# Optimization experiments

Measured on AMD Instinct MI355X. Metric: run time of the kernel, lower is better.

## Reference

```python
import jax, jax.numpy as jnp
import numpy as np

N_NODES = 50000
N_EDGES = 600000
D = 128
OUT = 16


def setup_inputs() -> dict:
    key = jax.random.key(0)
    k1, k2, k3, k4, k5, k6 = jax.random.split(key, 6)
    hn = jax.random.normal(k1, (N_NODES, D), dtype=jnp.float32)
    he = jax.random.normal(k2, (N_EDGES, D), dtype=jnp.float32)
    src = jax.random.randint(k3, (N_EDGES,), 0, N_NODES, dtype=jnp.int64)
    dst = jax.random.randint(k4, (N_EDGES,), 0, N_NODES, dtype=jnp.int64)
    W = jax.random.normal(k5, (OUT, 3 * D), dtype=jnp.float32) * 0.05
    b = jax.random.normal(k6, (OUT,), dtype=jnp.float32) * 0.05
    return {"hn": hn, "he": he, "src": src, "dst": dst, "W": W, "b": b}


def reference(hn, he, src, dst, W, b):
    # gather source/dest node features per edge, concat with edge feature
    h_u = hn[src]                      # [E, D]
    h_v = hn[dst]                      # [E, D]
    cat = jnp.concatenate([h_u, h_v, he], axis=1)  # [E, 3D]
    score = cat @ W.T + b              # [E, OUT]
    return score
```

## Files before the change

### kernel.cpp

```cpp
#include <hip/hip_runtime.h>
#include <hip/hip_bf16.h>


#define D      128
#define OUT    16
#define KTOT   384
#define KSTEPS 12

typedef __attribute__((ext_vector_type(8))) short  short8;
typedef __attribute__((ext_vector_type(4))) float  float4v;

__device__ __forceinline__ unsigned short f2bf(float x) {
    unsigned u = __builtin_bit_cast(unsigned, x);
    unsigned r = u + 0x7fffu + ((u >> 16) & 1u);
    return (unsigned short)(r >> 16);
}

__device__ __forceinline__ short8 load_cvt8(const float* __restrict__ p) {
    float4v a = *(const float4v*)(p);
    float4v c = *(const float4v*)(p + 4);
    short8 r;
#pragma unroll
    for (int i = 0; i < 4; ++i) {
        r[i]     = (short)f2bf(a[i]);
        r[i + 4] = (short)f2bf(c[i]);
    }
    return r;
}

__global__ __launch_bounds__(256) void egat_mfma_kernel(
    const float* __restrict__ hn,
    const float* __restrict__ he,
    const int*   __restrict__ src,
    const int*   __restrict__ dst,
    const float* __restrict__ W,
    const float* __restrict__ b,
    float*       __restrict__ out,
    int n_tiles, int total_waves)
{
    const int wave = (blockIdx.x * blockDim.x + threadIdx.x) >> 6;
    const int lane = threadIdx.x & 63;
    const int l    = lane & 15;
    const int quad = lane >> 4;
    const int off  = quad * 8;

    short8 wf[KSTEPS];
    const float* wrow = W + l * KTOT;
#pragma unroll
    for (int s = 0; s < KSTEPS; ++s)
        wf[s] = load_cvt8(wrow + s * 32 + off);

    const float bias = b[l];

    for (int tile = wave; tile < n_tiles; tile += total_waves) {
        const int e  = tile * 16 + l;
        const int su = src[e];
        const int dv = dst[e];
        const float* ru = hn + (size_t)su * D;
        const float* rv = hn + (size_t)dv * D;
        const float* re = he + (size_t)e  * D;

        float4v acc = {0.f, 0.f, 0.f, 0.f};
#pragma unroll
        for (int s = 0; s < 4; ++s) {
            short8 af = load_cvt8(ru + s * 32 + off);
            acc = __builtin_amdgcn_mfma_f32_16x16x32_bf16(af, wf[s], acc, 0, 0, 0);
        }
#pragma unroll
        for (int s = 0; s < 4; ++s) {
            short8 af = load_cvt8(rv + s * 32 + off);
            acc = __builtin_amdgcn_mfma_f32_16x16x32_bf16(af, wf[4 + s], acc, 0, 0, 0);
        }
#pragma unroll
        for (int s = 0; s < 4; ++s) {
            short8 af = load_cvt8(re + s * 32 + off);
            acc = __builtin_amdgcn_mfma_f32_16x16x32_bf16(af, wf[8 + s], acc, 0, 0, 0);
        }

        const size_t ebase = (size_t)tile * 16;
#pragma unroll
        for (int i = 0; i < 4; ++i) {
            int row = quad * 4 + i;
            out[(ebase + row) * OUT + l] = acc[i] + bias;
        }
    }
}

extern "C" void kernel_launch(void* const* d_in, const int* in_sizes, int n_in,
                              void* d_out, int out_size, void* d_ws, size_t ws_size,
                              hipStream_t stream) {
    const float* hn  = (const float*)d_in[0];
    const float* he  = (const float*)d_in[1];
    const int*   src = (const int*)d_in[2];
    const int*   dst = (const int*)d_in[3];
    const float* W   = (const float*)d_in[4];
    const float* b   = (const float*)d_in[5];
    float* out = (float*)d_out;

    const int E = in_sizes[2];
    const int n_tiles = E / 16;
    const int blocks = 1875;
    const int total_waves = blocks * 4;

    egat_mfma_kernel<<<blocks, 256, 0, stream>>>(hn, he, src, dst, W, b, out,
                                                 n_tiles, total_waves);
}
```

Baseline: 491.2 us.

## Stream edge features via async global-to-LDS copies and stage W in LDS

Each wave now copies its 16 contiguous edge-feature rows into padded LDS with asynchronous global_load_lds while it gathers and multiplies the node features. The next tile's src/dst indices are prefetched, and W is converted to bf16 once per block and held in LDS instead of registers. The grid becomes contiguous chunks of three tiles per wave. The aim is coalesced he loads, overlap of memory latency with MFMA work, and lower register pressure; the costs are LDS traffic for W and a hand-coded waitcnt whose correctness depends on the vmcnt encoding.

Result: faster. 475.9 us (-3.1%).

```diff
diff --git a/kernel.cpp b/kernel.cpp
--- a/kernel.cpp
+++ b/kernel.cpp
@@ -5,7 +5,10 @@
 #define D      128
 #define OUT    16
 #define KTOT   384
-#define KSTEPS 12
+#define HE_ROW_B   528
+#define HE_ROW_F   132
+#define HE_WAVE_F  2304
+#define W_ROW_S    392
 
 typedef __attribute__((ext_vector_type(8))) short  short8;
 typedef __attribute__((ext_vector_type(4))) float  float4v;
@@ -16,9 +19,7 @@
     return (unsigned short)(r >> 16);
 }
 
-__device__ __forceinline__ short8 load_cvt8(const float* __restrict__ p) {
-    float4v a = *(const float4v*)(p);
-    float4v c = *(const float4v*)(p + 4);
+__device__ __forceinline__ short8 cvt8(float4v a, float4v c) {
     short8 r;
 #pragma unroll
     for (int i = 0; i < 4; ++i) {
@@ -26,6 +27,12 @@
         r[i + 4] = (short)f2bf(c[i]);
     }
     return r;
+}
+
+__device__ __forceinline__ void async_copy16(const float* g, float* lds) {
+    __builtin_amdgcn_global_load_lds(
+        (const __attribute__((address_space(1))) void*)g,
+        (__attribute__((address_space(3))) void*)lds, 16, 0, 0);
 }
 
 __global__ __launch_bounds__(256) void egat_mfma_kernel(
@@ -36,53 +43,99 @@
     const float* __restrict__ W,
     const float* __restrict__ b,
     float*       __restrict__ out,
-    int n_tiles, int total_waves)
+    int n_tiles, int tiles_per_wave)
 {
-    const int wave = (blockIdx.x * blockDim.x + threadIdx.x) >> 6;
-    const int lane = threadIdx.x & 63;
+    __shared__ __align__(16) unsigned short w_lds[16 * W_ROW_S];
+    __shared__ __align__(16) float he_lds[4 * HE_WAVE_F];
+
+    const int tid  = threadIdx.x;
+    const int wib  = tid >> 6;
+    const int lane = tid & 63;
     const int l    = lane & 15;
     const int quad = lane >> 4;
     const int off  = quad * 8;
 
-    short8 wf[KSTEPS];
-    const float* wrow = W + l * KTOT;
+    for (int i = tid; i < 16 * KTOT; i += 256) {
+        int row = i / KTOT, col = i - row * KTOT;
+        w_lds[row * W_ROW_S + col] = f2bf(W[i]);
+    }
+    __syncthreads();
+
+    int goff[9];
 #pragma unroll
-    for (int s = 0; s < KSTEPS; ++s)
-        wf[s] = load_cvt8(wrow + s * 32 + off);
+    for (int j = 0; j < 9; ++j) {
+        int x = j * 1024 + lane * 16;
+        int r = x / HE_ROW_B;
+        int c = x - r * HE_ROW_B;
+        goff[j] = (r < 16 && c < 512) ? (r * 512 + c) >> 2 : 0;
+    }
 
     const float bias = b[l];
+    float* hb = &he_lds[wib * HE_WAVE_F];
 
-    for (int tile = wave; tile < n_tiles; tile += total_waves) {
-        const int e  = tile * 16 + l;
-        const int su = src[e];
-        const int dv = dst[e];
+    const int wave  = (blockIdx.x * 4) + wib;
+    const int tile0 = wave * tiles_per_wave;
+
+    int e0 = tile0 * 16 + l;
+    int su = src[e0];
+    int dv = dst[e0];
+
+    for (int i = 0; i < tiles_per_wave; ++i) {
+        const int tile = tile0 + i;
+        if (tile >= n_tiles) break;
+
+        const float* hp = he + (size_t)tile * (16 * D);
+#pragma unroll
+        for (int j = 0; j < 9; ++j)
+            async_copy16(hp + goff[j], hb + j * 256);
+
+        int tn = tile + 1; if (tn >= n_tiles) tn = n_tiles - 1;
+        const int en = tn * 16 + l;
+        const int su_n = src[en];
+        const int dv_n = dst[en];
+
         const float* ru = hn + (size_t)su * D;
         const float* rv = hn + (size_t)dv * D;
-        const float* re = he + (size_t)e  * D;
+        float4v au[8], av[8];
+#pragma unroll
+        for (int s = 0; s < 4; ++s) {
+            au[2 * s]     = *(const float4v*)(ru + s * 32 + off);
+            au[2 * s + 1] = *(const float4v*)(ru + s * 32 + off + 4);
+            av[2 * s]     = *(const float4v*)(rv + s * 32 + off);
+            av[2 * s + 1] = *(const float4v*)(rv + s * 32 + off + 4);
+        }
 
         float4v acc = {0.f, 0.f, 0.f, 0.f};
 #pragma unroll
         for (int s = 0; s < 4; ++s) {
-            short8 af = load_cvt8(ru + s * 32 + off);
-            acc = __builtin_amdgcn_mfma_f32_16x16x32_bf16(af, wf[s], acc, 0, 0, 0);
+            short8 wf = *(const short8*)&w_lds[l * W_ROW_S + s * 32 + off];
+            acc = __builtin_amdgcn_mfma_f32_16x16x32_bf16(
+                      cvt8(au[2 * s], au[2 * s + 1]), wf, acc, 0, 0, 0);
         }
 #pragma unroll
         for (int s = 0; s < 4; ++s) {
-            short8 af = load_cvt8(rv + s * 32 + off);
-            acc = __builtin_amdgcn_mfma_f32_16x16x32_bf16(af, wf[4 + s], acc, 0, 0, 0);
+            short8 wf = *(const short8*)&w_lds[l * W_ROW_S + (4 + s) * 32 + off];
+            acc = __builtin_amdgcn_mfma_f32_16x16x32_bf16(
+                      cvt8(av[2 * s], av[2 * s + 1]), wf, acc, 0, 0, 0);
         }
+
+        __builtin_amdgcn_s_waitcnt(0x0F70);
+
 #pragma unroll
         for (int s = 0; s < 4; ++s) {
-            short8 af = load_cvt8(re + s * 32 + off);
-            acc = __builtin_amdgcn_mfma_f32_16x16x32_bf16(af, wf[8 + s], acc, 0, 0, 0);
+            const int fi = l * HE_ROW_F + s * 32 + off;
+            float4v ha = *(const float4v*)&hb[fi];
+            float4v hc = *(const float4v*)&hb[fi + 4];
+            short8 wf = *(const short8*)&w_lds[l * W_ROW_S + (8 + s) * 32 + off];
+            acc = __builtin_amdgcn_mfma_f32_16x16x32_bf16(cvt8(ha, hc), wf, acc, 0, 0, 0);
         }
 
         const size_t ebase = (size_t)tile * 16;
 #pragma unroll
-        for (int i = 0; i < 4; ++i) {
-            int row = quad * 4 + i;
-            out[(ebase + row) * OUT + l] = acc[i] + bias;
-        }
+        for (int r = 0; r < 4; ++r)
+            out[(ebase + quad * 4 + r) * OUT + l] = acc[r] + bias;
+
+        su = su_n; dv = dv_n;
     }
 }
 
@@ -98,10 +151,11 @@
     float* out = (float*)d_out;
 
     const int E = in_sizes[2];
-    const int n_tiles = E / 16;
-    const int blocks = 1875;
-    const int total_waves = blocks * 4;
+    const int n_tiles = (E + 15) / 16;
+    const int tiles_per_wave = 3;
+    const int waves = (n_tiles + tiles_per_wave - 1) / tiles_per_wave;
+    const int blocks = (waves + 3) / 4;
 
     egat_mfma_kernel<<<blocks, 256, 0, stream>>>(hn, he, src, dst, W, b, out,
-                                                 n_tiles, total_waves);
+                                                 n_tiles, tiles_per_wave);
 }
```

## Precompute per-node projections, then gather projected scores per edge

Applied to the files above, without the earlier changes.

Splits the linear layer so each node's features are projected once through the src and dst slices of W into 16-wide vectors stored in workspace. The edge kernel then only runs the MFMA on the edge features and gathers two 16-float projections per edge instead of two 128-float node rows. This removes most of the random gather traffic in exchange for an extra launch and a workspace round trip. Edge tiles are also assigned in contiguous chunks per wave rather than grid-strided. The node kernel has no bounds check when N is not a multiple of 16, which does not arise for the given N.

Measured after the change: 446.3 us. 9.2% less time.

```diff
diff --git a/kernel.cpp b/kernel.cpp
--- a/kernel.cpp
+++ b/kernel.cpp
@@ -2,10 +2,9 @@
 #include <hip/hip_bf16.h>
 
 
-#define D      128
-#define OUT    16
-#define KTOT   384
-#define KSTEPS 12
+#define D   128
+#define OUT 16
+#define K3  384
 
 typedef __attribute__((ext_vector_type(8))) short  short8;
 typedef __attribute__((ext_vector_type(4))) float  float4v;
@@ -16,9 +15,7 @@
     return (unsigned short)(r >> 16);
 }
 
-__device__ __forceinline__ short8 load_cvt8(const float* __restrict__ p) {
-    float4v a = *(const float4v*)(p);
-    float4v c = *(const float4v*)(p + 4);
+__device__ __forceinline__ short8 cvt8(float4v a, float4v c) {
     short8 r;
 #pragma unroll
     for (int i = 0; i < 4; ++i) {
@@ -28,15 +25,63 @@
     return r;
 }
 
-__global__ __launch_bounds__(256) void egat_mfma_kernel(
+__device__ __forceinline__ short8 load_cvt8(const float* __restrict__ p) {
+    float4v a = *(const float4v*)(p);
+    float4v c = *(const float4v*)(p + 4);
+    return cvt8(a, c);
+}
+
+__global__ __launch_bounds__(256) void node_proj_kernel(
     const float* __restrict__ hn,
+    const float* __restrict__ W,
+    const float* __restrict__ b,
+    float*       __restrict__ Pu,
+    float*       __restrict__ Pv,
+    int n_tiles)
+{
+    const int wave = (blockIdx.x * blockDim.x + threadIdx.x) >> 6;
+    if (wave >= n_tiles) return;
+    const int lane = threadIdx.x & 63;
+    const int l    = lane & 15;
+    const int quad = lane >> 4;
+    const int off  = quad * 8;
+
+    short8 wu[4], wv[4];
+    const float* wrow = W + l * K3;
+#pragma unroll
+    for (int s = 0; s < 4; ++s) {
+        wu[s] = load_cvt8(wrow + s * 32 + off);
+        wv[s] = load_cvt8(wrow + D + s * 32 + off);
+    }
+    const float bias = b[l];
+
+    const int nbase = wave * 16;
+    const float* rn = hn + (size_t)(nbase + l) * D;
+    float4v accu = {0.f, 0.f, 0.f, 0.f};
+    float4v accv = {0.f, 0.f, 0.f, 0.f};
+#pragma unroll
+    for (int s = 0; s < 4; ++s) {
+        short8 af = load_cvt8(rn + s * 32 + off);
+        accu = __builtin_amdgcn_mfma_f32_16x16x32_bf16(af, wu[s], accu, 0, 0, 0);
+        accv = __builtin_amdgcn_mfma_f32_16x16x32_bf16(af, wv[s], accv, 0, 0, 0);
+    }
+#pragma unroll
+    for (int r = 0; r < 4; ++r) {
+        const int n = nbase + quad * 4 + r;
+        Pu[n * OUT + l] = accu[r] + bias;
+        Pv[n * OUT + l] = accv[r];
+    }
+}
+
+__global__ __launch_bounds__(256) void edge_score_kernel(
     const float* __restrict__ he,
     const int*   __restrict__ src,
     const int*   __restrict__ dst,
     const float* __restrict__ W,
-    const float* __restrict__ b,
+    const float* __restrict__ Pu,
+    const float* __restrict__ Pv,
     float*       __restrict__ out,
-    int n_tiles, int total_waves)
+    int n_tiles, int tiles_per_wave)
 {
     const int wave = (blockIdx.x * blockDim.x + threadIdx.x) >> 6;
     const int lane = threadIdx.x & 63;
@@ -44,45 +89,49 @@
     const int quad = lane >> 4;
     const int off  = quad * 8;
 
-    short8 wf[KSTEPS];
-    const float* wrow = W + l * KTOT;
+    short8 wf[4];
+    const float* wrow = W + l * K3 + 2 * D;
 #pragma unroll
-    for (int s = 0; s < KSTEPS; ++s)
+    for (int s = 0; s < 4; ++s)
         wf[s] = load_cvt8(wrow + s * 32 + off);
 
-    const float bias = b[l];
+    const int tile0 = wave * tiles_per_wave;
+    for (int i = 0; i < tiles_per_wave; ++i) {
+        const int tile = tile0 + i;
+        if (tile >= n_tiles) break;
+        const int ebase = tile * 16;
 
-    for (int tile = wave; tile < n_tiles; tile += total_waves) {
-        const int e  = tile * 16 + l;
-        const int su = src[e];
-        const int dv = dst[e];
-        const float* ru = hn + (size_t)su * D;
-        const float* rv = hn + (size_t)dv * D;
-        const float* re = he + (size_t)e  * D;
+        int su[4], dv[4];
+#pragma unroll
+        for (int r = 0; r < 4; ++r) {
+            su[r] = src[ebase + quad * 4 + r];
+            dv[r] = dst[ebase + quad * 4 + r];
+        }
+
+        const float* re = he + (size_t)(ebase + l) * D;
+        float4v ha[4], hc[4];
+#pragma unroll
+        for (int s = 0; s < 4; ++s) {
+            ha[s] = *(const float4v*)(re + s * 32 + off);
+            hc[s] = *(const float4v*)(re + s * 32 + off + 4);
+        }
+
+        float pu[4], pv[4];
+#pragma unroll
+        for (int r = 0; r < 4; ++r) {
+            pu[r] = Pu[(size_t)su[r] * OUT + l];
+            pv[r] = Pv[(size_t)dv[r] * OUT + l];
+        }
 
         float4v acc = {0.f, 0.f, 0.f, 0.f};
 #pragma unroll
-        for (int s = 0; s < 4; ++s) {
-            short8 af = load_cvt8(ru + s * 32 + off);
-            acc = __builtin_amdgcn_mfma_f32_16x16x32_bf16(af, wf[s], acc, 0, 0, 0);
-        }
+        for (int s = 0; s < 4; ++s)
+            acc = __builtin_amdgcn_mfma_f32_16x16x32_bf16(
+                      cvt8(ha[s], hc[s]), wf[s], acc, 0, 0, 0);
+
 #pragma unroll
-        for (int s = 0; s < 4; ++s) {
-            short8 af = load_cvt8(rv + s * 32 + off);
-            acc = __builtin_amdgcn_mfma_f32_16x16x32_bf16(af, wf[4 + s], acc, 0, 0, 0);
-        }
-#pragma unroll
-        for (int s = 0; s < 4; ++s) {
-            short8 af = load_cvt8(re + s * 32 + off);
-            acc = __builtin_amdgcn_mfma_f32_16x16x32_bf16(af, wf[8 + s], acc, 0, 0, 0);
-        }
-
-        const size_t ebase = (size_t)tile * 16;
-#pragma unroll
-        for (int i = 0; i < 4; ++i) {
-            int row = quad * 4 + i;
-            out[(ebase + row) * OUT + l] = acc[i] + bias;
-        }
+        for (int r = 0; r < 4; ++r)
+            out[(size_t)(ebase + quad * 4 + r) * OUT + l] = acc[r] + pu[r] + pv[r];
     }
 }
 
@@ -97,11 +146,20 @@
     const float* b   = (const float*)d_in[5];
     float* out = (float*)d_out;
 
+    const int N = in_sizes[0] / D;
     const int E = in_sizes[2];
-    const int n_tiles = E / 16;
-    const int blocks = 1875;
-    const int total_waves = blocks * 4;
 
-    egat_mfma_kernel<<<blocks, 256, 0, stream>>>(hn, he, src, dst, W, b, out,
-                                                 n_tiles, total_waves);
+    float* Pu = (float*)d_ws;
+    float* Pv = (float*)d_ws + (size_t)N * OUT;
+
+    const int nt_node = (N + 15) / 16;
+    const int blk1 = (nt_node + 3) / 4;
+    node_proj_kernel<<<blk1, 256, 0, stream>>>(hn, W, b, Pu, Pv, nt_node);
+
+    const int nt_edge = (E + 15) / 16;
+    const int tpw = 4;
+    const int waves = (nt_edge + tpw - 1) / tpw;
+    const int blk2 = (waves + 3) / 4;
+    edge_score_kernel<<<blk2, 256, 0, stream>>>(he, src, dst, W, Pu, Pv, out,
+                                                nt_edge, tpw);
 }
```
